# Kernel tuning notes

Hardware: AMD Instinct MI355X
Metric: run time of the kernel (lower is better)

## Reference

```python
import jax, jax.numpy as jnp
import numpy as np

B, D, NB = 262144, 64, 1000


def setup_inputs() -> dict:
    key = jax.random.key(0)
    k1, k2, k3, k4 = jax.random.split(key, 4)
    x = jax.random.normal(k1, (B, D), dtype=jnp.float32)
    # per-dim sorted grid (mimics fit_marginals' linspace over extended data range)
    lo = -3.0 + 0.5 * jax.random.normal(k2, (D, 1))
    hi = 3.0 + 0.5 * jax.random.normal(k3, (D, 1))
    t = jnp.linspace(0.0, 1.0, NB, dtype=jnp.float32)[None, :]
    x_values = (lo + (hi - lo) * t).astype(jnp.float32)  # [D, NB], sorted per row
    # strictly increasing empirical CDF in (1e-6, 1-1e-6)
    w = jax.nn.softmax(jax.random.normal(k4, (D, NB)), axis=1)
    cdf = jnp.cumsum(w, axis=1)
    cdf = jnp.clip(cdf / cdf[:, -1:], 1e-6, 1.0 - 1e-6).astype(jnp.float32)
    return {"x": x, "x_values": x_values, "cdf_values": cdf}


def reference(x, x_values, cdf_values):
    """MarginalGaussianization.forward: per-dim CDF lookup + Phi^{-1}, with log-det."""
    nb = x_values.shape[1]
    xT = x.T  # [D, B]
    # vectorized per-dim binary search (replaces the Python loop over dims)
    idx = jax.vmap(lambda xv, xd: jnp.searchsorted(xv, xd, side='left'))(x_values, xT)
    idx = jnp.clip(idx, 1, nb - 1)  # [D, B]
    g = lambda tab, i: jnp.take_along_axis(tab, i, axis=1)
    x_l, x_r = g(x_values, idx - 1), g(x_values, idx)
    c_l, c_r = g(cdf_values, idx - 1), g(cdf_values, idx)
    denom = x_r - x_l + 1e-12
    u = c_l + (c_r - c_l) * (xT - x_l) / denom          # _cdf_and_pdf: no weight clamp
    p_hat = jnp.maximum((c_r - c_l) / denom, 1e-12)
    u = jnp.clip(u, 1e-6, 1.0 - 1e-6)
    # inverse Gaussian CDF
    e = jnp.clip(2.0 * u - 1.0, -0.99999, 0.99999)
    z = jnp.clip(jnp.sqrt(2.0) * jax.scipy.special.erfinv(e), -10.0, 10.0)  # [D, B]
    inv_sqrt_2pi = 1.0 / jnp.sqrt(2.0 * jnp.pi)
    phi = inv_sqrt_2pi * jnp.exp(-0.5 * z * z)
    log_det = jnp.sum(jnp.log(p_hat) - jnp.log(phi + 1e-12), axis=0)  # [B]
    return z.T, log_det
```

## Files before the change

### kernel.cpp

```cpp
#include <hip/hip_runtime.h>
#include <math.h>

#define NBINS 1000
#define NDIM 64
#define DIMS_PER_BLOCK 8
#define DIM_GROUPS (NDIM / DIMS_PER_BLOCK)
#define BLOCK_THREADS 1024
#define ROWS_PER_ITER (BLOCK_THREADS / 2)
#define ROW_BLOCKS 128

__global__ __launch_bounds__(1024) void mg_zero(float* __restrict__ p, int n) {
    int i = blockIdx.x * blockDim.x + threadIdx.x;
    if (i < n) p[i] = 0.0f;
}

__global__ __launch_bounds__(256) void mg_reduce(const float* __restrict__ ws,
                                                 float* __restrict__ out, int B) {
    int row = blockIdx.x * blockDim.x + threadIdx.x;
    if (row >= B) return;
    float s = 0.0f;
#pragma unroll
    for (int g = 0; g < DIM_GROUPS; ++g) s += ws[(size_t)g * B + row];
    out[row] = s;
}

#define DIM_MATH(xd_, base_, i_, a_, b_, sc_, php_, ss_, zout_)                   \
    {                                                                             \
        float xd = (xd_);                                                         \
        int i = (i_);                                                             \
        float2 a = (a_), b = (b_);                                                \
        if (__builtin_expect((xd > b.x && i < NBINS - 2) ||                       \
                             (xd <= a.x && i > 0), 0)) {                          \
            while (xd > b.x && i < NBINS - 2) {                                   \
                ++i; a = b; b = knots[(base_) + i + 1];                           \
            }                                                                     \
            while (xd <= a.x && i > 0) {                                          \
                --i; b = a; a = knots[(base_) + i];                               \
            }                                                                     \
        }                                                                         \
        float slope = (b.y - a.y) * (sc_);                                        \
        float u = fmaf(slope, xd - a.x, a.y);                                     \
        float ph = fmaxf(slope, 1e-12f);                                          \
        u = fminf(fmaxf(u, 1e-6f), 1.0f - 1e-6f);                                 \
        float e1 = fminf(fmaxf(fmaf(2.0f, u, -1.0f), -0.99999f), 0.99999f);       \
        float wv = -0.6931471805599453f *                                         \
                   __builtin_amdgcn_logf(fmaf(-e1, e1, 1.0f));                    \
        float t = wv - 2.5f;                                                      \
        float p = 2.81022636e-08f;                                                \
        p = fmaf(p, t, 3.43273939e-07f);                                          \
        p = fmaf(p, t, -3.5233877e-06f);                                          \
        p = fmaf(p, t, -4.39150654e-06f);                                         \
        p = fmaf(p, t, 0.00021858087f);                                           \
        p = fmaf(p, t, -0.00125372503f);                                          \
        p = fmaf(p, t, -0.00417768164f);                                          \
        p = fmaf(p, t, 0.246640727f);                                             \
        p = fmaf(p, t, 1.50140941f);                                              \
        if (wv >= 5.0f) {                                                         \
            float tq = sqrtf(wv) - 3.0f;                                          \
            float pt = -0.000200214257f;                                          \
            pt = fmaf(pt, tq, 0.000100950558f);                                   \
            pt = fmaf(pt, tq, 0.00134934322f);                                    \
            pt = fmaf(pt, tq, -0.00367342844f);                                   \
            pt = fmaf(pt, tq, 0.00573950773f);                                    \
            pt = fmaf(pt, tq, -0.0076224613f);                                    \
            pt = fmaf(pt, tq, 0.00943887047f);                                    \
            pt = fmaf(pt, tq, 1.00167406f);                                       \
            pt = fmaf(pt, tq, 2.83297682f);                                       \
            p = pt;                                                               \
        }                                                                         \
        float z = 1.4142135623730951f * p * e1;   \
        (zout_) = z;                                                              \
        (ss_) = fmaf(z, z, (ss_));                                                \
        (php_) *= ph;                                                             \
    }

template <bool USE_WS>
__global__ __launch_bounds__(BLOCK_THREADS, 8)
void mg_main(const float* __restrict__ x,
             const float* __restrict__ xvals,
             const float* __restrict__ cdf,
             float* __restrict__ out, float* __restrict__ ws, int B) {
    __shared__ float2 knots[DIMS_PER_BLOCK * NBINS];

    const int dimbase = blockIdx.y * DIMS_PER_BLOCK;

    {
        const float4* xv4 = (const float4*)(xvals + (size_t)dimbase * NBINS);
        const float4* cd4 = (const float4*)(cdf + (size_t)dimbase * NBINS);
        for (int k = threadIdx.x; k < DIMS_PER_BLOCK * NBINS / 4; k += BLOCK_THREADS) {
            float4 a = xv4[k], c = cd4[k];
            knots[k * 4 + 0] = make_float2(a.x, c.x);
            knots[k * 4 + 1] = make_float2(a.y, c.y);
            knots[k * 4 + 2] = make_float2(a.z, c.z);
            knots[k * 4 + 3] = make_float2(a.w, c.w);
        }
    }
    __syncthreads();

    const int dl = (threadIdx.x & 1) * 4;
    const int qidx = blockIdx.y * 2 + (threadIdx.x & 1);

    float scale[4], bias[4];
#pragma unroll
    for (int j = 0; j < 4; ++j) {
        float l = knots[(dl + j) * NBINS].x;
        float h = knots[(dl + j) * NBINS + NBINS - 1].x;
        float s = (float)(NBINS - 1) / (h - l);
        scale[j] = s;
        bias[j] = -l * s;
    }

    const int rstride = gridDim.x * ROWS_PER_ITER;
    int row = blockIdx.x * ROWS_PER_ITER + (threadIdx.x >> 1);

    float4 xq = make_float4(0.f, 0.f, 0.f, 0.f);
    if (row < B) xq = ((const float4*)x)[(size_t)row * (NDIM / 4) + qidx];

    int ii[4];
    float2 kl[4], kr[4];
    {
        float xv[4] = {xq.x, xq.y, xq.z, xq.w};
#pragma unroll
        for (int j = 0; j < 4; ++j) {
            int i = (int)fmaf(xv[j], scale[j], bias[j]);
            ii[j] = min(max(i, 0), NBINS - 2);
        }
#pragma unroll
        for (int j = 0; j < 4; ++j) {
            kl[j] = knots[(dl + j) * NBINS + ii[j]];
            kr[j] = knots[(dl + j) * NBINS + ii[j] + 1];
        }
    }

    for (; row < B; row += rstride) {
        const int nrow = row + rstride;
        float4 xn = make_float4(0.f, 0.f, 0.f, 0.f);
        if (nrow < B) xn = ((const float4*)x)[(size_t)nrow * (NDIM / 4) + qidx];

        float z4[4], php = 1.0f, sumsq = 0.0f;
        DIM_MATH(xq.x, (dl + 0) * NBINS, ii[0], kl[0], kr[0], scale[0],
                 php, sumsq, z4[0]);
        DIM_MATH(xq.y, (dl + 1) * NBINS, ii[1], kl[1], kr[1], scale[1],
                 php, sumsq, z4[1]);
        DIM_MATH(xq.z, (dl + 2) * NBINS, ii[2], kl[2], kr[2], scale[2],
                 php, sumsq, z4[2]);
        DIM_MATH(xq.w, (dl + 3) * NBINS, ii[3], kl[3], kr[3], scale[3],
                 php, sumsq, z4[3]);

        {
            float xv[4] = {xn.x, xn.y, xn.z, xn.w};
#pragma unroll
            for (int j = 0; j < 4; ++j) {
                int i = (int)fmaf(xv[j], scale[j], bias[j]);
                ii[j] = min(max(i, 0), NBINS - 2);
            }
#pragma unroll
            for (int j = 0; j < 4; ++j) {
                kl[j] = knots[(dl + j) * NBINS + ii[j]];
                kr[j] = knots[(dl + j) * NBINS + ii[j] + 1];
            }
        }

        ((float4*)out)[(size_t)row * (NDIM / 4) + qidx] =
            make_float4(z4[0], z4[1], z4[2], z4[3]);

        float term = fmaf(0.5f, sumsq, 4.0f * 0.9189385332046727f) +
                     0.6931471805599453f * __builtin_amdgcn_logf(php);

        term += __shfl_xor(term, 1, 64);
        if ((threadIdx.x & 1) == 0) {
            if constexpr (USE_WS)
                ws[(size_t)blockIdx.y * B + row] = term;
            else
                atomicAdd(out + (size_t)B * NDIM + row, term);
        }

        xq = xn;
    }
}

extern "C" void kernel_launch(void* const* d_in, const int* in_sizes, int n_in,
                              void* d_out, int out_size, void* d_ws, size_t ws_size,
                              hipStream_t stream) {
    const float* x = (const float*)d_in[0];
    const float* xvals = (const float*)d_in[1];
    const float* cdf = (const float*)d_in[2];
    float* out = (float*)d_out;
    int B = in_sizes[0] / NDIM;

    const size_t ws_need = (size_t)DIM_GROUPS * B * sizeof(float);
    dim3 grid(ROW_BLOCKS, DIM_GROUPS);

    if (ws_size >= ws_need) {
        float* ws = (float*)d_ws;
        hipLaunchKernelGGL((mg_main<true>), grid, dim3(BLOCK_THREADS), 0, stream,
                           x, xvals, cdf, out, ws, B);
        hipLaunchKernelGGL(mg_reduce, dim3((B + 255) / 256), dim3(256), 0, stream,
                           ws, out + (size_t)B * NDIM, B);
    } else {
        hipLaunchKernelGGL(mg_zero, dim3((B + 1023) / 1024), dim3(1024), 0, stream,
                           out + (size_t)B * NDIM, B);
        hipLaunchKernelGGL((mg_main<false>), grid, dim3(BLOCK_THREADS), 0, stream,
                           x, xvals, cdf, out, (float*)nullptr, B);
    }
}
```

Before: 144.1 us.

## Store knot pairs as float4 quads and halve dims per block

Each shared-memory entry now holds a float4 with both knot endpoints (x_l, c_l, x_r, c_r), so one LDS read per dimension replaces two float2 reads. Each block now covers 4 dimensions instead of 8, with each thread doing 2 dimensions via float2 loads, which doubles the block-grid along the dimension axis. The software prefetch of the next row's knots is dropped. The trade-off is twice the shared-memory bytes per dimension, more blocks reloading the tables, more partial log-det sums to reduce, and less per-thread ILP.

```diff
diff --git a/kernel.cpp b/kernel.cpp
--- a/kernel.cpp
+++ b/kernel.cpp
@@ -3,7 +3,7 @@
 
 #define NBINS 1000
 #define NDIM 64
-#define DIMS_PER_BLOCK 8
+#define DIMS_PER_BLOCK 4
 #define DIM_GROUPS (NDIM / DIMS_PER_BLOCK)
 #define BLOCK_THREADS 1024
 #define ROWS_PER_ITER (BLOCK_THREADS / 2)
@@ -24,22 +24,18 @@
     out[row] = s;
 }
 
-#define DIM_MATH(xd_, base_, i_, a_, b_, sc_, php_, ss_, zout_)                   \
+#define QDIM_MATH(xd_, base_, i_, q_, sc_, php_, ss_, zout_)                      \
     {                                                                             \
         float xd = (xd_);                                                         \
         int i = (i_);                                                             \
-        float2 a = (a_), b = (b_);                                                \
-        if (__builtin_expect((xd > b.x && i < NBINS - 2) ||                       \
-                             (xd <= a.x && i > 0), 0)) {                          \
-            while (xd > b.x && i < NBINS - 2) {                                   \
-                ++i; a = b; b = knots[(base_) + i + 1];                           \
-            }                                                                     \
-            while (xd <= a.x && i > 0) {                                          \
-                --i; b = a; a = knots[(base_) + i];                               \
-            }                                                                     \
+        float4 q = (q_);                                                          \
+        if (__builtin_expect((xd > q.z && i < NBINS - 2) ||                       \
+                             (xd <= q.x && i > 0), 0)) {                          \
+            while (xd > q.z && i < NBINS - 2) { ++i; q = quads[(base_) + i]; }    \
+            while (xd <= q.x && i > 0) { --i; q = quads[(base_) + i]; }           \
         }                                                                         \
-        float slope = (b.y - a.y) * (sc_);                                        \
-        float u = fmaf(slope, xd - a.x, a.y);                                     \
+        float slope = (q.w - q.y) * (sc_);                                        \
+        float u = fmaf(slope, xd - q.x, q.y);                                     \
         float ph = fmaxf(slope, 1e-12f);                                          \
         u = fminf(fmaxf(u, 1e-6f), 1.0f - 1e-6f);                                 \
         float e1 = fminf(fmaxf(fmaf(2.0f, u, -1.0f), -0.99999f), 0.99999f);       \
@@ -80,91 +76,60 @@
              const float* __restrict__ xvals,
              const float* __restrict__ cdf,
              float* __restrict__ out, float* __restrict__ ws, int B) {
-    __shared__ float2 knots[DIMS_PER_BLOCK * NBINS];
+    __shared__ float4 quads[DIMS_PER_BLOCK * NBINS];
 
     const int dimbase = blockIdx.y * DIMS_PER_BLOCK;
 
-    {
-        const float4* xv4 = (const float4*)(xvals + (size_t)dimbase * NBINS);
-        const float4* cd4 = (const float4*)(cdf + (size_t)dimbase * NBINS);
-        for (int k = threadIdx.x; k < DIMS_PER_BLOCK * NBINS / 4; k += BLOCK_THREADS) {
-            float4 a = xv4[k], c = cd4[k];
-            knots[k * 4 + 0] = make_float2(a.x, c.x);
-            knots[k * 4 + 1] = make_float2(a.y, c.y);
-            knots[k * 4 + 2] = make_float2(a.z, c.z);
-            knots[k * 4 + 3] = make_float2(a.w, c.w);
+#pragma unroll
+    for (int d = 0; d < DIMS_PER_BLOCK; ++d) {
+        const float* xv = xvals + (size_t)(dimbase + d) * NBINS;
+        const float* cv = cdf + (size_t)(dimbase + d) * NBINS;
+        for (int i = threadIdx.x; i < NBINS; i += BLOCK_THREADS) {
+            int ip = (i < NBINS - 1) ? i + 1 : i;
+            quads[d * NBINS + i] = make_float4(xv[i], cv[i], xv[ip], cv[ip]);
         }
     }
     __syncthreads();
 
-    const int dl = (threadIdx.x & 1) * 4;
+    const int dl = (threadIdx.x & 1) * 2;
+    const int base0 = dl * NBINS, base1 = base0 + NBINS;
     const int qidx = blockIdx.y * 2 + (threadIdx.x & 1);
 
-    float scale[4], bias[4];
-#pragma unroll
-    for (int j = 0; j < 4; ++j) {
-        float l = knots[(dl + j) * NBINS].x;
-        float h = knots[(dl + j) * NBINS + NBINS - 1].x;
-        float s = (float)(NBINS - 1) / (h - l);
-        scale[j] = s;
-        bias[j] = -l * s;
+    float scale0, bias0, scale1, bias1;
+    {
+        float l0 = quads[base0].x, h0 = quads[base0 + NBINS - 2].z;
+        float l1 = quads[base1].x, h1 = quads[base1 + NBINS - 2].z;
+        scale0 = (float)(NBINS - 1) / (h0 - l0);
+        bias0 = -l0 * scale0;
+        scale1 = (float)(NBINS - 1) / (h1 - l1);
+        bias1 = -l1 * scale1;
     }
 
     const int rstride = gridDim.x * ROWS_PER_ITER;
     int row = blockIdx.x * ROWS_PER_ITER + (threadIdx.x >> 1);
 
-    float4 xq = make_float4(0.f, 0.f, 0.f, 0.f);
-    if (row < B) xq = ((const float4*)x)[(size_t)row * (NDIM / 4) + qidx];
-
-    int ii[4];
-    float2 kl[4], kr[4];
-    {
-        float xv[4] = {xq.x, xq.y, xq.z, xq.w};
-#pragma unroll
-        for (int j = 0; j < 4; ++j) {
-            int i = (int)fmaf(xv[j], scale[j], bias[j]);
-            ii[j] = min(max(i, 0), NBINS - 2);
-        }
-#pragma unroll
-        for (int j = 0; j < 4; ++j) {
-            kl[j] = knots[(dl + j) * NBINS + ii[j]];
-            kr[j] = knots[(dl + j) * NBINS + ii[j] + 1];
-        }
-    }
+    float2 xq = make_float2(0.f, 0.f);
+    if (row < B) xq = ((const float2*)x)[(size_t)row * (NDIM / 2) + qidx];
 
     for (; row < B; row += rstride) {
         const int nrow = row + rstride;
-        float4 xn = make_float4(0.f, 0.f, 0.f, 0.f);
-        if (nrow < B) xn = ((const float4*)x)[(size_t)nrow * (NDIM / 4) + qidx];
+        float2 xn = make_float2(0.f, 0.f);
+        if (nrow < B) xn = ((const float2*)x)[(size_t)nrow * (NDIM / 2) + qidx];
 
-        float z4[4], php = 1.0f, sumsq = 0.0f;
-        DIM_MATH(xq.x, (dl + 0) * NBINS, ii[0], kl[0], kr[0], scale[0],
-                 php, sumsq, z4[0]);
-        DIM_MATH(xq.y, (dl + 1) * NBINS, ii[1], kl[1], kr[1], scale[1],
-                 php, sumsq, z4[1]);
-        DIM_MATH(xq.z, (dl + 2) * NBINS, ii[2], kl[2], kr[2], scale[2],
-                 php, sumsq, z4[2]);
-        DIM_MATH(xq.w, (dl + 3) * NBINS, ii[3], kl[3], kr[3], scale[3],
-                 php, sumsq, z4[3]);
+        int i0 = (int)fmaf(xq.x, scale0, bias0);
+        int i1 = (int)fmaf(xq.y, scale1, bias1);
+        i0 = min(max(i0, 0), NBINS - 2);
+        i1 = min(max(i1, 0), NBINS - 2);
+        float4 q0 = quads[base0 + i0];
+        float4 q1 = quads[base1 + i1];
 
-        {
-            float xv[4] = {xn.x, xn.y, xn.z, xn.w};
-#pragma unroll
-            for (int j = 0; j < 4; ++j) {
-                int i = (int)fmaf(xv[j], scale[j], bias[j]);
-                ii[j] = min(max(i, 0), NBINS - 2);
-            }
-#pragma unroll
-            for (int j = 0; j < 4; ++j) {
-                kl[j] = knots[(dl + j) * NBINS + ii[j]];
-                kr[j] = knots[(dl + j) * NBINS + ii[j] + 1];
-            }
-        }
+        float z0, z1, php = 1.0f, sumsq = 0.0f;
+        QDIM_MATH(xq.x, base0, i0, q0, scale0, php, sumsq, z0);
+        QDIM_MATH(xq.y, base1, i1, q1, scale1, php, sumsq, z1);
 
-        ((float4*)out)[(size_t)row * (NDIM / 4) + qidx] =
-            make_float4(z4[0], z4[1], z4[2], z4[3]);
+        ((float2*)out)[(size_t)row * (NDIM / 2) + qidx] = make_float2(z0, z1);
 
-        float term = fmaf(0.5f, sumsq, 4.0f * 0.9189385332046727f) +
+        float term = fmaf(0.5f, sumsq, 2.0f * 0.9189385332046727f) +
                      0.6931471805599453f * __builtin_amdgcn_logf(php);
 
         term += __shfl_xor(term, 1, 64);
```

Result: slower. 183.7 us (+27.4%).
